# Kernel optimization log

Measured on AMD Instinct MI355X. Metric: run time of the kernel, lower is better.

Reference implementation:

```python
import jax, jax.numpy as jnp
import numpy as np

D = 128           # embed_dim
NUM_LAYERS = 2
N_CLASSES = 4
OUT_CELL = 64
SPEAKERS = 2
INPUT_DIMS = [768, 74, 35]
B, T = 32, 60


def setup_inputs() -> dict:
    key = jax.random.key(0)
    ks = jax.random.split(key, 24)
    inp = {}
    inp['x0'] = jax.random.normal(ks[0], (B, T, INPUT_DIMS[0]), jnp.float32)
    inp['x1'] = jax.random.normal(ks[1], (B, T, INPUT_DIMS[1]), jnp.float32)
    inp['x2'] = jax.random.normal(ks[2], (B, T, INPUT_DIMS[2]), jnp.float32)
    inp['smask'] = jax.random.normal(ks[3], (B, T, SPEAKERS), jnp.float32)  # argmax -> speaker ids
    # modality projections
    for i, d in enumerate(INPUT_DIMS):
        inp[f'Wp{i}'] = jax.random.normal(ks[4 + i], (d, D), jnp.float32) / np.float32(np.sqrt(d))
        inp[f'bp{i}'] = jnp.zeros((D,), jnp.float32)
    # shared PositionEmbedding (ModuleList([m]*3) shares params)
    inp['freq_emb'] = jax.random.normal(ks[7], (SPEAKERS, D), jnp.float32) * 0.1
    inp['phase_emb'] = jax.random.normal(ks[8], (SPEAKERS, D), jnp.float32)
    # shared QRNNCell (ModuleList([cell]*num_layers) shares params)
    inp['U_x'] = jnp.linalg.qr(jax.random.normal(ks[9], (D, D), jnp.float32))[0]
    inp['U_h'] = jnp.linalg.qr(jax.random.normal(ks[10], (D, D), jnp.float32))[0]
    inp['Lambda'] = jnp.float32(0.5)
    # QMeasurement kernel (real/imag parts of D measurement vectors)
    inp['kernel_r'] = jnp.eye(D, dtype=jnp.float32) + 0.05 * jax.random.normal(ks[11], (D, D), jnp.float32)
    inp['kernel_i'] = 0.05 * jax.random.normal(ks[12], (D, D), jnp.float32)
    # SimpleNet fc_out
    inp['W1'] = jax.random.normal(ks[13], (D, OUT_CELL), jnp.float32) / np.float32(np.sqrt(D))
    inp['b1'] = jnp.zeros((OUT_CELL,), jnp.float32)
    inp['W2'] = jax.random.normal(ks[14], (OUT_CELL, N_CLASSES), jnp.float32) / np.float32(np.sqrt(OUT_CELL))
    inp['b2'] = jnp.zeros((N_CLASSES,), jnp.float32)
    return inp


def _qmn_forward(x0, x1, x2, smask, Wp0, bp0, Wp1, bp1, Wp2, bp2,
                 freq_emb, phase_emb, U_x, U_h, Lambda,
                 kernel_r, kernel_i, W1, b1, W2, b2):
    xs = [x0, x1, x2]
    Ws = [(Wp0, bp0), (Wp1, bp1), (Wp2, bp2)]
    reps = [jax.nn.relu(x @ W + b) for x, (W, b) in zip(xs, Ws)]           # [B,T,D] each
    # mixture weights: softmax over per-modality L2 norms
    norms = jnp.concatenate([jnp.linalg.norm(r, axis=-1, keepdims=True) for r in reps], axis=-1)
    weights = jax.nn.softmax(norms, axis=-1)                               # [B,T,M]
    # shared phase embedding: phase = t * freq[speaker] + phase[speaker]
    ids = jnp.argmax(smask, axis=-1)                                       # [B,T] int
    pos = jnp.arange(T, dtype=jnp.float32)[None, :, None]                  # [1,T,1]
    phase = pos * freq_emb[ids] + phase_emb[ids]                           # [B,T,D]
    cosp, sinp = jnp.cos(phase), jnp.sin(phase)
    # mixed density matrices rho = sum_m w_m |v_m><v_m|
    rho_r = jnp.zeros((B, T, D, D), jnp.float32)
    rho_i = jnp.zeros((B, T, D, D), jnp.float32)
    for m, r in enumerate(reps):
        a = r / jnp.maximum(jnp.linalg.norm(r, axis=-1, keepdims=True), 1e-12)
        pr = a * cosp                                                       # real amplitude
        pi = a * sinp                                                       # imag amplitude
        w = weights[..., m][..., None, None]
        rho_r = rho_r + w * (jnp.einsum('btm,btn->btmn', pr, pr) + jnp.einsum('btm,btn->btmn', pi, pi))
        rho_i = rho_i + w * (jnp.einsum('btm,btn->btmn', pi, pr) - jnp.einsum('btm,btn->btmn', pr, pi))
    # time-major for scan
    sr = jnp.transpose(rho_r, (1, 0, 2, 3))                                # [T,B,D,D]
    si = jnp.transpose(rho_i, (1, 0, 2, 3))

    def cell(h, x):
        hr, hi = h
        xr, xi = x
        Xr = jnp.einsum('mp,bpq,nq->bmn', U_x, xr, U_x)
        Xi = jnp.einsum('mp,bpq,nq->bmn', U_x, xi, U_x)
        Hr = jnp.einsum('mp,bpq,nq->bmn', U_h, hr, U_h)
        Hi = jnp.einsum('mp,bpq,nq->bmn', U_h, hi, U_h)
        nr = Lambda * Hr + (1.0 - Lambda) * Xr
        ni = Lambda * Hi + (1.0 - Lambda) * Xi
        return (nr, ni), (nr, ni)

    h0 = (jnp.broadcast_to(jnp.eye(D, dtype=jnp.float32) / D, (B, D, D)),
          jnp.zeros((B, D, D), jnp.float32))
    for _ in range(NUM_LAYERS):  # same shared cell params each layer
        _, (sr, si) = jax.lax.scan(cell, h0, (sr, si))
    # QMeasurement: p_k = Re(v_k^dag rho v_k), unit-norm complex measurement vectors
    nrm = jnp.sqrt(jnp.sum(kernel_r**2 + kernel_i**2, axis=1, keepdims=True))
    vr = kernel_r / jnp.maximum(nrm, 1e-12)                                # [K,D], K=D
    vi = kernel_i / jnp.maximum(nrm, 1e-12)
    probs = (jnp.einsum('tbmn,km,kn->tbk', sr, vr, vr)
             + jnp.einsum('tbmn,km,kn->tbk', sr, vi, vi)
             - jnp.einsum('tbmn,km,kn->tbk', si, vr, vi)
             + jnp.einsum('tbmn,km,kn->tbk', si, vi, vr))                  # [T,B,D]
    # SimpleNet (dropout = identity at inference)
    hid = jax.nn.relu(probs @ W1 + b1)
    out = jnp.tanh(hid @ W2 + b2)                                          # [T,B,C]
    out = jnp.transpose(out, (1, 0, 2))                                    # [B,T,C]
    return jax.nn.log_softmax(out, axis=2)


def reference(x0, x1, x2, smask, Wp0, bp0, Wp1, bp1, Wp2, bp2,
              freq_emb, phase_emb, U_x, U_h, Lambda,
              kernel_r, kernel_i, W1, b1, W2, b2):
    return _qmn_forward(x0, x1, x2, smask, Wp0, bp0, Wp1, bp1, Wp2, bp2,
                        freq_emb, phase_emb, U_x, U_h, Lambda,
                        kernel_r, kernel_i, W1, b1, W2, b2)
```

## Files before the change

kernel.cpp:

```cpp
#include <hip/hip_runtime.h>


#define DB 32
#define DT 60
#define DD 128
#define BT (DB*DT)
#define SP 136

typedef unsigned short ushort_t;
typedef __attribute__((ext_vector_type(8))) __bf16 bf16x8;
typedef __attribute__((ext_vector_type(8))) unsigned short ushort8_t;
typedef __attribute__((ext_vector_type(4))) float  float4v;

__device__ __forceinline__ float bf2f(ushort_t u){
  union { unsigned int i; float f; } x; x.i = ((unsigned int)u) << 16; return x.f;
}
__device__ __forceinline__ ushort_t f2bf(float f){
  union { float f; unsigned int i; } x; x.f = f;
  unsigned int lsb = (x.i >> 16) & 1u;
  return (ushort_t)((x.i + 0x7FFFu + lsb) >> 16);
}
__device__ __forceinline__ unsigned int f2bfpk(float a, float b){
#if defined(__gfx950__) && __has_builtin(__builtin_amdgcn_cvt_pk_bf16_f32)
  auto v = __builtin_amdgcn_cvt_pk_bf16_f32(a, b);
  unsigned int r; __builtin_memcpy(&r, &v, 4); return r;
#else
  return (unsigned int)f2bf(a) | ((unsigned int)f2bf(b) << 16);
#endif
}
__device__ __forceinline__ void split2(float v, ushort_t& h, ushort_t& l){
  h = f2bf(v); l = f2bf(v - bf2f(h));
}

template<int RT, int CT, bool ALO, bool BLO>
__device__ __forceinline__ void gemm_t(const ushort_t* Ah, const ushort_t* Al,
                                       const ushort_t* Bh, const ushort_t* Bl,
                                       float4v* acc, int row0, int col0, int gma, int q)
{
  for (int ks = 0; ks < 4; ks++){
    int ko = ks*32 + q*8;
    bf16x8 aF[RT], aL[RT], bF[CT], bL[CT];
    #pragma unroll
    for (int R = 0; R < RT; R++){
      int row = row0 + 16*R + gma;
      aF[R] = *(const bf16x8*)&Ah[row*SP + ko];
      if (ALO) aL[R] = *(const bf16x8*)&Al[row*SP + ko];
    }
    #pragma unroll
    for (int C = 0; C < CT; C++){
      int row = col0 + 16*C + gma;
      bF[C] = *(const bf16x8*)&Bh[row*SP + ko];
      if (BLO) bL[C] = *(const bf16x8*)&Bl[row*SP + ko];
    }
    #pragma unroll
    for (int R = 0; R < RT; R++)
      #pragma unroll
      for (int C = 0; C < CT; C++){
        float4v c = acc[R*CT+C];
        c = __builtin_amdgcn_mfma_f32_16x16x32_bf16(aF[R], bF[C], c, 0, 0, 0);
        if (BLO) c = __builtin_amdgcn_mfma_f32_16x16x32_bf16(aF[R], bL[C], c, 0, 0, 0);
        if (ALO) c = __builtin_amdgcn_mfma_f32_16x16x32_bf16(aL[R], bF[C], c, 0, 0, 0);
        acc[R*CT+C] = c;
      }
  }
}

template<int RT, int CT>
__device__ __forceinline__ void emit_t(const float4v* acc, ushort_t* dst, int stride,
                                       int row0, int col0, int gma, int q){
  #pragma unroll
  for (int R = 0; R < RT; R++)
    #pragma unroll
    for (int C = 0; C < CT; C++){
      int c = col0 + 16*C + gma, r0 = row0 + 16*R + 4*q;
      uint2 o;
      o.x = f2bfpk(acc[R*CT+C][0], acc[R*CT+C][1]);
      o.y = f2bfpk(acc[R*CT+C][2], acc[R*CT+C][3]);
      *(uint2*)&dst[(size_t)c*stride + r0] = o;
    }
}
template<int RT, int CT>
__device__ __forceinline__ void emit_split_t(const float4v* acc, ushort_t* dh, ushort_t* dl, int stride,
                                             int row0, int col0, int gma, int q){
  #pragma unroll
  for (int R = 0; R < RT; R++)
    #pragma unroll
    for (int C = 0; C < CT; C++){
      int c = col0 + 16*C + gma, r0 = row0 + 16*R + 4*q;
      ushort4 hh, ll;
      split2(acc[R*CT+C][0], hh.x, ll.x); split2(acc[R*CT+C][1], hh.y, ll.y);
      split2(acc[R*CT+C][2], hh.z, ll.z); split2(acc[R*CT+C][3], hh.w, ll.w);
      *(ushort4*)&dh[(size_t)c*stride + r0] = hh;
      *(ushort4*)&dl[(size_t)c*stride + r0] = ll;
    }
}
template<int NT>
__device__ __forceinline__ void lds_load_mat(ushort_t* dst, const ushort_t* src, int tid){
  for (int i = tid*8; i < 16384; i += NT*8){
    int r = i >> 7, k = i & 127;
    *(ushort8_t*)&dst[r*SP + k] = *(const ushort8_t*)&src[i];
  }
}
template<int NT>
__device__ __forceinline__ void lds_load_rows16(ushort_t* dst, const ushort_t* src, int tid){
  for (int i = tid*8; i < 2048; i += NT*8){
    int r = i >> 7, k = i & 127;
    *(ushort8_t*)&dst[r*SP + k] = *(const ushort8_t*)&src[i];
  }
}
template<int NT>
__device__ __forceinline__ void lds_load_mat2(ushort_t* d0, const ushort_t* s0,
                                              ushort_t* d1, const ushort_t* s1, int tid){
  constexpr int CH = 16384/(NT*8);
  ushort8_t r0[CH], r1[CH];
  #pragma unroll
  for (int c = 0; c < CH; c++) r0[c] = *(const ushort8_t*)&s0[tid*8 + c*NT*8];
  #pragma unroll
  for (int c = 0; c < CH; c++) r1[c] = *(const ushort8_t*)&s1[tid*8 + c*NT*8];
  #pragma unroll
  for (int c = 0; c < CH; c++){
    int i = tid*8 + c*NT*8; int r = i >> 7, k = i & 127;
    *(ushort8_t*)&d0[r*SP + k] = r0[c];
  }
  #pragma unroll
  for (int c = 0; c < CH; c++){
    int i = tid*8 + c*NT*8; int r = i >> 7, k = i & 127;
    *(ushort8_t*)&d1[r*SP + k] = r1[c];
  }
}
template<int NT>
__device__ __forceinline__ void lds_store_mat(ushort_t* dst, const ushort_t* src, int tid){
  for (int i = tid*8; i < 16384; i += NT*8){
    int r = i >> 7, k = i & 127;
    *(ushort8_t*)&dst[i] = *(const ushort8_t*)&src[r*SP + k];
  }
}

__device__ __forceinline__ void pow2_body(int blk2, int s,
    ushort_t* PpH, ushort_t* PpL, ushort_t* PTh, ushort_t* PTl,
    int tid, ushort_t* Ah, ushort_t* Al, ushort_t* Bh, ushort_t* Bl)
{
  int which = blk2 >> 3, sl = blk2 & 7;
  size_t src = (size_t)(s-1)*16384, dst = (size_t)s*16384;
  int gcol0 = sl*16;
  const ushort_t *A_h, *A_l, *B_h, *B_l; ushort_t *D_h, *D_l;
  if (which == 0){ A_h = PTh+src; A_l = PTl+src; B_h = PpH+src; B_l = PpL+src;
                   D_h = PpH+dst; D_l = PpL+dst; }
  else           { A_h = PpH+src; A_l = PpL+src; B_h = PTh+src; B_l = PTl+src;
                   D_h = PTh+dst; D_l = PTl+dst; }
  if (tid < 256){
    lds_load_mat<256>(Ah, A_h, tid);
    lds_load_mat<256>(Al, A_l, tid);
    lds_load_rows16<256>(Bh, B_h + (size_t)gcol0*128, tid);
    lds_load_rows16<256>(Bl, B_l + (size_t)gcol0*128, tid);
  }
  __syncthreads();
  if (tid < 256){
    int w = tid >> 6, lane = tid & 63, gma = lane & 15, q = lane >> 4;
    int row0 = 32*w;
    float4v acc[2];
    acc[0] = (float4v){0.f,0.f,0.f,0.f};
    acc[1] = (float4v){0.f,0.f,0.f,0.f};
    gemm_t<2,1,true,true>(Ah, Al, Bh, Bl, acc, row0, 0, gma, q);
    emit_split_t<2,1>(acc, D_h, D_l, 128, row0, gcol0, gma, q);
  }
}

__global__ void k_small(const float* Ux, const float* Uh, const float* kr, const float* ki,
                        const float* Wp0, const float* Wp1, const float* Wp2,
                        const float* x0, const float* x1, const float* x2,
                        ushort_t* UxTh, ushort_t* UxTl, ushort_t* UxH, ushort_t* UxL,
                        float* Vr, float* Vi,
                        ushort_t* PpH, ushort_t* PpL, ushort_t* PTh, ushort_t* PTl,
                        ushort_t* WT0h, ushort_t* WT0l, ushort_t* WT1h, ushort_t* WT1l,
                        ushort_t* WT2h, ushort_t* WT2l,
                        ushort_t* X0h, ushort_t* X0l, ushort_t* X1h, ushort_t* X1l,
                        ushort_t* X2h, ushort_t* X2l){
  int blk = blockIdx.x, d = threadIdx.x;
  if (blk < 128){
    int i = blk;
    float v = Ux[i*DD + d];
    ushort_t h, l; split2(v, h, l);
    UxTh[d*DD + i] = h; UxTl[d*DD + i] = l;
  } else if (blk < 256){
    __shared__ float red[DD];
    int k = blk - 128;
    float r = kr[k*DD+d], im = ki[k*DD+d];
    red[d] = r*r + im*im;
    __syncthreads();
    for (int s = 64; s > 0; s >>= 1){ if (d < s) red[d] += red[d+s]; __syncthreads(); }
    float nrm = fmaxf(sqrtf(red[0]), 1e-12f);
    Vr[k*DD+d] = r/nrm; Vi[k*DD+d] = im/nrm;
  } else if (blk < 384){
    int i = blk - 256;
    float v = Uh[i*DD + d];
    ushort_t h, l; split2(v, h, l);
    PpH[i*DD + d] = h;  PpL[i*DD + d] = l;
    PTh[d*DD + i] = h;  PTl[d*DD + i] = l;
  } else if (blk < 512){
    int dd2 = blk - 384;
    ushort_t h, l;
    for (int k = d; k < 768; k += 128){
      split2(Wp0[(size_t)k*DD + dd2], h, l);
      WT0h[(size_t)dd2*768 + k] = h; WT0l[(size_t)dd2*768 + k] = l;
    }
    { float v = (d < 74) ? Wp1[(size_t)d*DD + dd2] : 0.f;
      split2(v, h, l); WT1h[dd2*128 + d] = h; WT1l[dd2*128 + d] = l; }
    { float v = (d < 35) ? Wp2[(size_t)d*DD + dd2] : 0.f;
      split2(v, h, l); WT2h[dd2*128 + d] = h; WT2l[dd2*128 + d] = l; }
    { split2(Ux[(size_t)dd2*DD + d], h, l);
      UxH[dd2*DD + d] = h; UxL[dd2*DD + d] = l; }
  } else {
    int bt = blk - 512;
    ushort_t h, l;
    const float* r0 = x0 + (size_t)bt*768;
    #pragma unroll
    for (int j = 0; j < 6; j++){
      split2(r0[j*128 + d], h, l);
      X0h[(size_t)bt*768 + j*128 + d] = h;
      X0l[(size_t)bt*768 + j*128 + d] = l;
    }
    float v1 = (d < 74) ? x1[(size_t)bt*74 + d] : 0.f;
    split2(v1, h, l);
    X1h[(size_t)bt*128 + d] = h; X1l[(size_t)bt*128 + d] = l;
    float v2 = (d < 35) ? x2[(size_t)bt*35 + d] : 0.f;
    split2(v2, h, l);
    X2h[(size_t)bt*128 + d] = h; X2l[(size_t)bt*128 + d] = l;
  }
}

__global__ __launch_bounds__(512,1) void k_proj(
    const ushort_t* X0h, const ushort_t* X0l, const ushort_t* X1h, const ushort_t* X1l,
    const ushort_t* X2h, const ushort_t* X2l,
    const ushort_t* WT0h, const ushort_t* WT0l, const ushort_t* WT1h, const ushort_t* WT1l,
    const ushort_t* WT2h, const ushort_t* WT2l,
    const float* bp1, const float* bp2,
    float* Rpart, float* Reps,
    ushort_t* PpH, ushort_t* PpL, ushort_t* PTh, ushort_t* PTl)
{
  __shared__ ushort_t Ah[128*SP], Al[128*SP], Bh[128*SP], Bl[128*SP];
  int blk = blockIdx.x;
  int tid = threadIdx.x;
  if (blk >= 120){
    pow2_body(blk - 120, 1, PpH, PpL, PTh, PTl, tid, Ah, Al, Bh, Bl);
    return;
  }
  int m, tile, ch;
  if (blk < 90){ m = 0; tile = blk/6; ch = blk%6; }
  else if (blk < 105){ m = 1; tile = blk-90; ch = 0; }
  else { m = 2; tile = blk-105; ch = 0; }
  int bt0 = tile*128;
  int w = tid >> 6, lane = tid & 63, gma = lane & 15, q = lane >> 4;
  int row0 = 32*(w >> 1), col0 = 64*(w & 1);
  const ushort_t* Wh_ = (m==0)? WT0h : (m==1)? WT1h : WT2h;
  const ushort_t* Wl_ = (m==0)? WT0l : (m==1)? WT1l : WT2l;
  const ushort_t* Xh_ = (m==0)? X0h : (m==1)? X1h : X2h;
  const ushort_t* Xl_ = (m==0)? X0l : (m==1)? X1l : X2l;
  int KX = (m==0)? 768 : 128;
  for (int i = tid*8; i < 16384; i += 4096){
    int r = i >> 7, k = i & 127;
    *(ushort8_t*)&Ah[r*SP + k] = *(const ushort8_t*)&Wh_[(size_t)r*KX + ch*128 + k];
    *(ushort8_t*)&Al[r*SP + k] = *(const ushort8_t*)&Wl_[(size_t)r*KX + ch*128 + k];
    *(ushort8_t*)&Bh[r*SP + k] = *(const ushort8_t*)&Xh_[(size_t)(bt0+r)*KX + ch*128 + k];
    *(ushort8_t*)&Bl[r*SP + k] = *(const ushort8_t*)&Xl_[(size_t)(bt0+r)*KX + ch*128 + k];
  }
  __syncthreads();
  float4v acc[8];
  #pragma unroll
  for (int i = 0; i < 8; i++) acc[i] = (float4v){0.f,0.f,0.f,0.f};
  gemm_t<2,4,true,true>(Ah, Al, Bh, Bl, acc, row0, col0, gma, q);
  if (m == 0){
    #pragma unroll
    for (int R = 0; R < 2; R++)
      #pragma unroll
      for (int C = 0; C < 4; C++){
        int c = col0 + 16*C + gma, r0 = row0 + 16*R + 4*q;
        float4 o;
        o.x = acc[R*4+C][0]; o.y = acc[R*4+C][1];
        o.z = acc[R*4+C][2]; o.w = acc[R*4+C][3];
        *(float4*)&Rpart[((size_t)ch*BT + bt0 + c)*128 + r0] = o;
      }
  } else {
    const float* bp = (m==1)? bp1 : bp2;
    #pragma unroll
    for (int R = 0; R < 2; R++){
      int r0 = row0 + 16*R + 4*q;
      float4 bv = *(const float4*)&bp[r0];
      #pragma unroll
      for (int C = 0; C < 4; C++){
        int c = col0 + 16*C + gma;
        float4v a = acc[R*4+C];
        float4 o;
        o.x = fmaxf(a[0]+bv.x, 0.f); o.y = fmaxf(a[1]+bv.y, 0.f);
        o.z = fmaxf(a[2]+bv.z, 0.f); o.w = fmaxf(a[3]+bv.w, 0.f);
        *(float4*)&Reps[(size_t)(bt0 + c)*384 + m*128 + r0] = o;
      }
    }
  }
}

__global__ __launch_bounds__(128) void k_mix(const float* Rpart, const float* Reps,
    const float* bp0, const float* smask,
    const float* freq, const float* phem, ushort_t* PsH, ushort_t* PsL, float* Wgt)
{
  __shared__ float part[2][3];
  int bt = blockIdx.x; int t = bt % DT;
  int d = threadIdx.x;
  float r0v = bp0[d];
  #pragma unroll
  for (int ch = 0; ch < 6; ch++)
    r0v += Rpart[((size_t)ch*BT + bt)*128 + d];
  r0v = fmaxf(r0v, 0.f);
  float r1v = Reps[(size_t)bt*384 + 128 + d];
  float r2v = Reps[(size_t)bt*384 + 256 + d];
  float s0 = r0v*r0v, s1 = r1v*r1v, s2 = r2v*r2v;
  #pragma unroll
  for (int off = 1; off < 64; off <<= 1){
    s0 += __shfl_xor(s0, off, 64);
    s1 += __shfl_xor(s1, off, 64);
    s2 += __shfl_xor(s2, off, 64);
  }
  int wv = d >> 6;
  if ((d & 63) == 0){ part[wv][0] = s0; part[wv][1] = s1; part[wv][2] = s2; }
  __syncthreads();
  float n0 = sqrtf(part[0][0] + part[1][0]);
  float n1 = sqrtf(part[0][1] + part[1][1]);
  float n2 = sqrtf(part[0][2] + part[1][2]);
  float mx = fmaxf(n0, fmaxf(n1, n2));
  float e0 = expf(n0-mx), e1 = expf(n1-mx), e2 = expf(n2-mx);
  float einv = 1.f/(e0+e1+e2);
  if (d < 3) Wgt[bt*3+d] = (d==0?e0:(d==1?e1:e2))*einv;
  float sm0 = smask[bt*2], sm1 = smask[bt*2+1];
  int id = (sm1 > sm0) ? 1 : 0;
  float ph = (float)t * freq[id*DD+d] + phem[id*DD+d];
  float cp = cosf(ph), sp = sinf(ph);
  float a0 = r0v / fmaxf(n0, 1e-12f);
  float a1 = r1v / fmaxf(n1, 1e-12f);
  float a2 = r2v / fmaxf(n2, 1e-12f);
  ushort_t h, l;
  split2(a0*cp, h, l); PsH[((size_t)0*BT + bt)*DD + d] = h; PsL[((size_t)0*BT + bt)*DD + d] = l;
  split2(a1*cp, h, l); PsH[((size_t)1*BT + bt)*DD + d] = h; PsL[((size_t)1*BT + bt)*DD + d] = l;
  split2(a2*cp, h, l); PsH[((size_t)2*BT + bt)*DD + d] = h; PsL[((size_t)2*BT + bt)*DD + d] = l;
  split2(a0*sp, h, l); PsH[((size_t)3*BT + bt)*DD + d] = h; PsL[((size_t)3*BT + bt)*DD + d] = l;
  split2(a1*sp, h, l); PsH[((size_t)4*BT + bt)*DD + d] = h; PsL[((size_t)4*BT + bt)*DD + d] = l;
  split2(a2*sp, h, l); PsH[((size_t)5*BT + bt)*DD + d] = h; PsL[((size_t)5*BT + bt)*DD + d] = l;
}

__global__ __launch_bounds__(512,1) void k_qtrans(const ushort_t* UxH, const ushort_t* UxL,
                                                  const ushort_t* PsH, const ushort_t* PsL,
                                                  ushort_t* Qb,
                                                  ushort_t* PpH, ushort_t* PpL,
                                                  ushort_t* PTh, ushort_t* PTl){
  __shared__ ushort_t Ah[128*SP], Al[128*SP], Bh[128*SP], Bl[128*SP];
  int blk = blockIdx.x;
  int tid = threadIdx.x;
  if (blk >= 90){
    pow2_body(blk - 90, 2, PpH, PpL, PTh, PTl, tid, Ah, Al, Bh, Bl);
    return;
  }
  int w = tid >> 6, lane = tid & 63, gma = lane & 15, q = lane >> 4;
  int row0 = 32*(w >> 1), col0 = 64*(w & 1);
  size_t rbase = (size_t)blk*128*128;
  lds_load_mat<512>(Ah, UxH, tid);
  lds_load_mat<512>(Al, UxL, tid);
  lds_load_mat<512>(Bh, PsH + rbase, tid);
  lds_load_mat<512>(Bl, PsL + rbase, tid);
  __syncthreads();
  float4v acc[8];
  #pragma unroll
  for (int i = 0; i < 8; i++) acc[i] = (float4v){0.f,0.f,0.f,0.f};
  gemm_t<2,4,true,true>(Ah, Al, Bh, Bl, acc, row0, col0, gma, q);
  emit_t<2,4>(acc, Qb + rbase, 128, row0, col0, gma, q);
}

__global__ __launch_bounds__(256,2) void k_pow2v2(ushort_t* PpH, ushort_t* PpL,
                                                  ushort_t* PTh, ushort_t* PTl, int s){
  __shared__ ushort_t Ah[128*SP], Al[128*SP], Bh[16*SP], Bl[16*SP];
  int blk = blockIdx.x;
  int which = blk >> 3, sl = blk & 7;
  size_t src = (size_t)(s-1)*16384, dst = (size_t)s*16384;
  int tid = threadIdx.x;
  int w = tid >> 6, lane = tid & 63, gma = lane & 15, q = lane >> 4;
  int row0 = 32*w;
  int gcol0 = sl*16;
  const ushort_t *A_h, *A_l, *B_h, *B_l; ushort_t *D_h, *D_l;
  if (which == 0){ A_h = PTh+src; A_l = PTl+src; B_h = PpH+src; B_l = PpL+src;
                   D_h = PpH+dst; D_l = PpL+dst; }
  else           { A_h = PpH+src; A_l = PpL+src; B_h = PTh+src; B_l = PTl+src;
                   D_h = PTh+dst; D_l = PTl+dst; }
  lds_load_mat<256>(Ah, A_h, tid);
  lds_load_mat<256>(Al, A_l, tid);
  lds_load_rows16<256>(Bh, B_h + (size_t)gcol0*128, tid);
  lds_load_rows16<256>(Bl, B_l + (size_t)gcol0*128, tid);
  __syncthreads();
  float4v acc[2];
  acc[0] = (float4v){0.f,0.f,0.f,0.f};
  acc[1] = (float4v){0.f,0.f,0.f,0.f};
  gemm_t<2,1,true,true>(Ah, Al, Bh, Bl, acc, row0, 0, gma, q);
  emit_split_t<2,1>(acc, D_h, D_l, 128, row0, gcol0, gma, q);
}

__global__ __launch_bounds__(512,1) void k_gchain(const ushort_t* PpH, const ushort_t* PpL,
                                                  const ushort_t* PTh, const ushort_t* PTl,
                                                  ushort_t* GTh, ushort_t* GTl){
  __shared__ ushort_t Ah[128*SP], Al[128*SP], Bh[128*SP], Bl[128*SP];
  int t = blockIdx.x;
  int tid = threadIdx.x;
  int w = tid >> 6, lane = tid & 63, gma = lane & 15, q = lane >> 4;
  int row0 = 32*(w >> 1), col0 = 64*(w & 1);
  size_t gslot = (size_t)t * 16384;
  if (t == 0){
    for (int i = tid*4; i < 16384; i += 2048){
      int r = i >> 7, k = i & 127;
      ushort4 zz; zz.x = zz.y = zz.z = zz.w = 0;
      *(ushort4*)&GTl[gslot + i] = zz;
      ushort4 oh;
      oh.x = (r == (k+0)) ? (ushort_t)0x3F80 : (ushort_t)0;
      oh.y = (r == (k+1)) ? (ushort_t)0x3F80 : (ushort_t)0;
      oh.z = (r == (k+2)) ? (ushort_t)0x3F80 : (ushort_t)0;
      oh.w = (r == (k+3)) ? (ushort_t)0x3F80 : (ushort_t)0;
      *(ushort4*)&GTh[gslot + i] = oh;
    }
    return;
  }
  int b0 = __ffs(t) - 1;
  int rem = t & ~(1 << b0);
  if (rem == 0){
    size_t ps = (size_t)b0 * 16384;
    for (int i = tid*4; i < 16384; i += 2048){
      *(ushort4*)&GTh[gslot + i] = *(const ushort4*)&PTh[ps + i];
      *(ushort4*)&GTl[gslot + i] = *(const ushort4*)&PTl[ps + i];
    }
    return;
  }
  lds_load_mat<512>(Ah, PpH + (size_t)b0*16384, tid);
  lds_load_mat<512>(Al, PpL + (size_t)b0*16384, tid);
  while (rem){
    int k = __ffs(rem) - 1;
    rem &= ~(1 << k);
    lds_load_mat<512>(Bh, PTh + (size_t)k*16384, tid);
    lds_load_mat<512>(Bl, PTl + (size_t)k*16384, tid);
    __syncthreads();
    float4v acc[8];
    #pragma unroll
    for (int i = 0; i < 8; i++) acc[i] = (float4v){0.f,0.f,0.f,0.f};
    if (rem){
      gemm_t<2,4,true,true>(Bh, Bl, Ah, Al, acc, row0, col0, gma, q);
      __syncthreads();
      emit_split_t<2,4>(acc, Ah, Al, SP, row0, col0, gma, q);
      __syncthreads();
    } else {
      gemm_t<2,4,true,true>(Ah, Al, Bh, Bl, acc, row0, col0, gma, q);
      emit_split_t<2,4>(acc, GTh + gslot, GTl + gslot, 128, row0, col0, gma, q);
    }
  }
}

__global__ __launch_bounds__(512,1) void k_mwvt(
    const ushort_t* GTh, const ushort_t* GTl,
    const ushort_t* UxTh, const ushort_t* UxTl,
    const float* Vr, const float* Vi,
    const ushort_t* Qb,
    ushort_t* Mh, ushort_t* Wh, ushort_t* At)
{
  __shared__ ushort_t LBUF[4*128*SP];
  int blk = blockIdx.x;
  int tid = threadIdx.x;
  if (blk < 180){
    ushort_t* Bh = LBUF;
    ushort_t* Bl = LBUF + 128*SP;
    ushort_t* Ah = LBUF + 2*128*SP;
    ushort_t* Al = LBUF + 3*128*SP;
    int w = tid >> 6, lane = tid & 63, gma = lane & 15, q = lane >> 4;
    int row0 = 64*(w >> 1), col0 = 64*(w & 1);
    if (blk < 60){
      int t = blk;
      if (tid < 256){
        lds_load_mat<256>(Bh, GTh + (size_t)t*16384, tid);
        lds_load_mat<256>(Bl, GTl + (size_t)t*16384, tid);
        lds_load_mat<256>(Ah, UxTh, tid);
        lds_load_mat<256>(Al, UxTl, tid);
      }
      __syncthreads();
      float4v acc[16];
      if (tid < 256){
        #pragma unroll
        for (int i = 0; i < 16; i++) acc[i] = (float4v){0.f,0.f,0.f,0.f};
        gemm_t<4,4,true,true>(Ah, Al, Bh, Bl, acc, row0, col0, gma, q);
      }
      __syncthreads();
      if (tid < 256) emit_split_t<4,4>(acc, Ah, Al, SP, row0, col0, gma, q);
      __syncthreads();
      if (tid < 256){
        #pragma unroll
        for (int i = 0; i < 16; i++) acc[i] = (float4v){0.f,0.f,0.f,0.f};
        gemm_t<4,4,true,true>(Bh, Bl, Ah, Al, acc, row0, col0, gma, q);
        #pragma unroll
        for (int R = 0; R < 4; R++)
          #pragma unroll
          for (int C = 0; C < 4; C++){
            int c = col0 + 16*C + gma, r0 = row0 + 16*R + 4*q;
            uint2 o;
            o.x = f2bfpk(acc[R*4+C][0], acc[R*4+C][1]);
            o.y = f2bfpk(acc[R*4+C][2], acc[R*4+C][3]);
            *(uint2*)&Mh[(size_t)t*16384 + c*128 + r0] = o;
          }
      }
    } else {
      int bx = blk - 60;
      int t = bx >> 1, which = bx & 1;
      if (tid < 256){
        lds_load_mat<256>(Ah, GTh + (size_t)t*16384, tid);
        lds_load_mat<256>(Al, GTl + (size_t)t*16384, tid);
        const float* V = which ? Vi : Vr;
        for (int i = tid; i < 16384; i += 256){
          int r = i >> 7, k = i & 127;
          ushort_t h, l; split2(V[i], h, l);
          Bh[r*SP + k] = h; Bl[r*SP + k] = l;
        }
      }
      __syncthreads();
      if (tid < 256){
        float4v acc[16];
        #pragma unroll
        for (int i = 0; i < 16; i++) acc[i] = (float4v){0.f,0.f,0.f,0.f};
        gemm_t<4,4,true,true>(Ah, Al, Bh, Bl, acc, row0, col0, gma, q);
        #pragma unroll
        for (int R = 0; R < 4; R++)
          #pragma unroll
          for (int C = 0; C < 4; C++){
            int c = col0 + 16*C + gma, r0 = row0 + 16*R + 4*q;
            uint2 o;
            o.x = f2bfpk(acc[R*4+C][0], acc[R*4+C][1]);
            o.y = f2bfpk(acc[R*4+C][2], acc[R*4+C][3]);
            *(uint2*)&Wh[(size_t)bx*16384 + c*128 + r0] = o;
          }
      }
    }
  } else {
    ushort_t* Ah = LBUF;
    ushort_t* Bs = LBUF + 128*SP;
    int t = blk - 180;
    int w = tid >> 6, lane = tid & 63, gma = lane & 15, q = lane >> 4;
    int row0 = (w & 3)*32, col0 = (w >> 2)*96;
    lds_load_mat<512>(Ah, GTh + (size_t)t*16384, tid);
    for (int i = tid*8; i < 192*128; i += 4096){
      int m = i >> 7, k = i & 127;
      int j = m >> 5, b = m & 31;
      *(ushort8_t*)&Bs[m*SP + k] =
        *(const ushort8_t*)&Qb[((size_t)(j*BT) + b*DT + t)*DD + k];
    }
    __syncthreads();
    float4v acc[12];
    #pragma unroll
    for (int i = 0; i < 12; i++) acc[i] = (float4v){0.f,0.f,0.f,0.f};
    gemm_t<2,6,false,false>(Ah, Ah, Bs, Bs, acc, row0, col0, gma, q);
    emit_t<2,6>(acc, At + (size_t)t*24576, 128, row0, col0, gma, q);
  }
}

__global__ __launch_bounds__(256) void k_zbuild(ushort_t* S, const ushort_t* At,
                                                const float* Wgt, const float* lamp){
  __shared__ ushort_t As[2][6*DD];
  __shared__ float wl[2][3];
  int blk = blockIdx.x;
  int b = blk >> 5, sl2 = blk & 31;
  int tid = threadIdx.x;
  int r = sl2*4 + (tid >> 6);
  int c = (tid*2) & 127;
  float lam = lamp[0];
  float z0 = 0.f, z1 = 0.f;
  size_t off = (size_t)sl2*512 + tid*2;
  ushort4 pre;
  float wpre = 0.f;
  int jj0 = 0, n0 = 0;
  if (tid < 192){
    int i = tid*4;
    jj0 = i >> 7; n0 = i & 127;
    pre = *(const ushort4*)&At[(size_t)(jj0*32 + b)*128 + n0];
  }
  if (tid < 3) wpre = Wgt[(b*DT)*3 + tid];
  for (int t = 0; t < DT; t++){
    int cur = t & 1;
    if (tid < 192) *(ushort4*)&As[cur][tid*4] = pre;
    if (tid < 3) wl[cur][tid] = wpre;
    __syncthreads();
    if (t+1 < DT){
      if (tid < 192)
        pre = *(const ushort4*)&At[(size_t)(t+1)*24576 + (size_t)(jj0*32 + b)*128 + n0];
      if (tid < 3) wpre = Wgt[(b*DT + t+1)*3 + tid];
    }
    float ar[6];
    #pragma unroll
    for (int jj = 0; jj < 6; jj++) ar[jj] = bf2f(As[cur][jj*128 + r]);
    float w0 = wl[cur][0], w1 = wl[cur][1], w2 = wl[cur][2];
    float cb[6];
    cb[0] = w0*(ar[0]+ar[3]); cb[1] = w1*(ar[1]+ar[4]); cb[2] = w2*(ar[2]+ar[5]);
    cb[3] = w0*(ar[3]-ar[0]); cb[4] = w1*(ar[4]-ar[1]); cb[5] = w2*(ar[5]-ar[2]);
    float y0 = 0.f, y1 = 0.f;
    #pragma unroll
    for (int jj = 0; jj < 6; jj++){
      unsigned int a2 = *(const unsigned int*)&As[cur][jj*128 + c];
      float w_ = cb[jj];
      y0 += w_*bf2f((ushort_t)(a2 & 0xFFFF));
      y1 += w_*bf2f((ushort_t)(a2 >> 16));
    }
    z0 = lam*z0 + y0; z1 = lam*z1 + y1;
    *(unsigned int*)&S[((size_t)(t*32 + b))*16384 + off] = f2bfpk(z0, z1);
  }
}

__global__ __launch_bounds__(512,2) void k_conjmid(ushort_t* S, const ushort_t* Mh,
                                                   const float* lamp){
  __shared__ ushort_t Bh[128*SP], Zs[128*SP];
  int raw = blockIdx.x;
  int g = raw & 7, t = raw >> 3;
  int tid = threadIdx.x;
  int w = tid >> 6, lane = tid & 63, gma = lane & 15, q = lane >> 4;
  int row0 = 32*(w >> 1), col0 = 64*(w & 1);
  size_t slot0 = (size_t)(t*32 + g*4) * 16384;
  lds_load_mat2<512>(Zs, S + slot0, Bh, Mh + (size_t)t*16384, tid);
  __syncthreads();
  float lam = lamp[0];
  float oml = 1.f - lam;
  float ct = powf(lam, (float)(t+1)) / 128.f;
  for (int ib = 0; ib < 4; ib++){
    size_t slot = slot0 + (size_t)ib*16384;
    ushort8_t znext[4];
    if (ib < 3){
      #pragma unroll
      for (int c = 0; c < 4; c++)
        znext[c] = *(const ushort8_t*)&S[slot + 16384 + tid*8 + c*4096];
    }
    float4v acc[8];
    #pragma unroll
    for (int i = 0; i < 8; i++) acc[i] = (float4v){0.f,0.f,0.f,0.f};
    gemm_t<2,4,false,false>(Zs, Zs, Bh, Bh, acc, row0, col0, gma, q);
    __syncthreads();
    emit_t<2,4>(acc, Zs, SP, row0, col0, gma, q);
    __syncthreads();
    #pragma unroll
    for (int i = 0; i < 8; i++) acc[i] = (float4v){0.f,0.f,0.f,0.f};
    gemm_t<2,4,false,false>(Zs, Zs, Bh, Bh, acc, row0, col0, gma, q);
    __syncthreads();
    #pragma unroll
    for (int R = 0; R < 2; R++)
      #pragma unroll
      for (int C = 0; C < 4; C++){
        int c = col0 + 16*C + gma, r0 = row0 + 16*R + 4*q;
        float v0 = oml*acc[R*4+C][0] + ((c == r0+0) ? ct : 0.f);
        float v1 = oml*acc[R*4+C][1] + ((c == r0+1) ? ct : 0.f);
        float v2 = oml*acc[R*4+C][2] + ((c == r0+2) ? ct : 0.f);
        float v3 = oml*acc[R*4+C][3] + ((c == r0+3) ? ct : 0.f);
        uint2 o; o.x = f2bfpk(v0, v1); o.y = f2bfpk(v2, v3);
        *(uint2*)&Zs[(size_t)c*SP + r0] = o;
      }
    __syncthreads();
    lds_store_mat<512>(S + slot, Zs, tid);
    if (ib < 3){
      __syncthreads();
      #pragma unroll
      for (int c = 0; c < 4; c++){
        int i = tid*8 + c*4096;
        int r = i >> 7, k = i & 127;
        *(ushort8_t*)&Zs[r*SP + k] = znext[c];
      }
      __syncthreads();
    }
  }
}

__device__ __forceinline__ void prefix_ph2(uint2& buf, bool doload,
                                           const ushort_t* Snext, ushort_t* Scur,
                                           float* a, float lam){
  uint2 u = buf;
  if (doload) buf = *(const uint2*)Snext;
  a[0] = lam*a[0] + bf2f((ushort_t)(u.x & 0xFFFF));
  a[1] = lam*a[1] + bf2f((ushort_t)(u.x >> 16));
  a[2] = lam*a[2] + bf2f((ushort_t)(u.y & 0xFFFF));
  a[3] = lam*a[3] + bf2f((ushort_t)(u.y >> 16));
  uint2 o;
  o.x = f2bfpk(a[0], a[1]); o.y = f2bfpk(a[2], a[3]);
  *(uint2*)Scur = o;
}
__global__ __launch_bounds__(128) void k_prefix(ushort_t* S, const float* lamp){
  int blk = blockIdx.x;
  int chain = blk >> 5, slab = blk & 31;
  int tid = threadIdx.x;
  size_t off = (size_t)slab*512 + tid*4;
  float lam = lamp[0];
  float a[4];
  #pragma unroll
  for (int i = 0; i < 4; i++) a[i] = 0.f;
  size_t addr = (size_t)chain*16384 + off;
  const size_t step = (size_t)32*16384;
  uint2 b0 = *(const uint2*)&S[addr];
  uint2 b1 = *(const uint2*)&S[addr + step];
  uint2 b2 = *(const uint2*)&S[addr + 2*step];
  uint2 b3 = *(const uint2*)&S[addr + 3*step];
  uint2 b4 = *(const uint2*)&S[addr + 4*step];
  uint2 b5 = *(const uint2*)&S[addr + 5*step];
  for (int t = 0; t < DT; t += 6){
    prefix_ph2(b0, t+6  < DT, &S[addr + 6*step], &S[addr], a, lam); addr += step;
    prefix_ph2(b1, t+7  < DT, &S[addr + 6*step], &S[addr], a, lam); addr += step;
    prefix_ph2(b2, t+8  < DT, &S[addr + 6*step], &S[addr], a, lam); addr += step;
    prefix_ph2(b3, t+9  < DT, &S[addr + 6*step], &S[addr], a, lam); addr += step;
    prefix_ph2(b4, t+10 < DT, &S[addr + 6*step], &S[addr], a, lam); addr += step;
    prefix_ph2(b5, t+11 < DT, &S[addr + 6*step], &S[addr], a, lam); addr += step;
  }
}

__global__ __launch_bounds__(512,2) void k_meas(const ushort_t* S, const ushort_t* Wh,
                                                const float* lamp, float* Probs){
  __shared__ ushort_t Vs[128*SP], Cs[128*SP];
  __shared__ float Pd[64];
  int raw = blockIdx.x;
  int h = raw / 240;
  int rem = raw % 240;
  int t = rem >> 2, g = rem & 3;
  int tid = threadIdx.x;
  int w = tid >> 6, lane = tid & 63, gma = lane & 15, q = lane >> 4;
  int row0 = 16*(w >> 1);
  int col0 = 64*(w & 1);
  size_t wbase = (size_t)(t*2) * 16384;
  size_t slot0 = (size_t)(t*32 + g*8) * 16384;
  ushort8_t creg[4], vreg[4];
  #pragma unroll
  for (int c = 0; c < 4; c++)
    creg[c] = *(const ushort8_t*)&S[slot0 + tid*8 + c*4096];
  #pragma unroll
  for (int c = 0; c < 4; c++){
    int i = tid*8 + c*4096;
    int r = i >> 7, k = i & 127;
    size_t gsrc = wbase + ((r < 64) ? 0 : 16384) + (size_t)(64*h + (r & 63))*128 + k;
    vreg[c] = *(const ushort8_t*)&Wh[gsrc];
  }
  if (tid < 64) Pd[tid] = 0.f;
  #pragma unroll
  for (int c = 0; c < 4; c++){
    int i = tid*8 + c*4096;
    int r = i >> 7, k = i & 127;
    *(ushort8_t*)&Cs[r*SP + k] = creg[c];
    *(ushort8_t*)&Vs[r*SP + k] = vreg[c];
  }
  __syncthreads();
  float lam = lamp[0];
  float ct = powf(lam, (float)(t+1)) / 128.f;
  for (int ib = 0; ib < 8; ib++){
    if (ib < 7){
      size_t snx = slot0 + (size_t)(ib+1)*16384;
      #pragma unroll
      for (int c = 0; c < 4; c++)
        creg[c] = *(const ushort8_t*)&S[snx + tid*8 + c*4096];
    }
    float4v acc[8];
    #pragma unroll
    for (int i = 0; i < 8; i++) acc[i] = (float4v){0.f,0.f,0.f,0.f};
    #pragma unroll
    for (int ks = 0; ks < 4; ks++){
      int ko = ks*32 + q*8;
      bf16x8 aF0 = *(const bf16x8*)&Vs[(row0 + gma)*SP + ko];
      bf16x8 aF1 = *(const bf16x8*)&Vs[(row0 + 64 + gma)*SP + ko];
      bf16x8 bF[4];
      #pragma unroll
      for (int C = 0; C < 4; C++)
        bF[C] = *(const bf16x8*)&Cs[(col0 + 16*C + gma)*SP + ko];
      #pragma unroll
      for (int C = 0; C < 4; C++){
        acc[C]   = __builtin_amdgcn_mfma_f32_16x16x32_bf16(aF0, bF[C], acc[C],   0, 0, 0);
        acc[4+C] = __builtin_amdgcn_mfma_f32_16x16x32_bf16(aF1, bF[C], acc[4+C], 0, 0, 0);
      }
    }
    #pragma unroll
    for (int j = 0; j < 4; j++){
      int kr = row0 + 4*q + j;
      float s = 0.f;
      #pragma unroll
      for (int C = 0; C < 4; C++){
        int m = col0 + 16*C + gma;
        float w0 = bf2f(Vs[kr*SP + m]);
        float w1 = bf2f(Vs[(kr + 64)*SP + m]);
        s += acc[C][j]*(w0 + w1) + acc[4+C][j]*(w1 - w0);
      }
      #pragma unroll
      for (int off = 1; off < 16; off <<= 1)
        s += __shfl_xor(s, off, 64);
      if (gma == 0) atomicAdd(&Pd[kr], s);
    }
    __syncthreads();
    if (tid < 64){
      Probs[(size_t)(t*32 + g*8 + ib)*DD + 64*h + tid] = (1.f - lam)*Pd[tid] + ct;
      Pd[tid] = 0.f;
    }
    if (ib < 7){
      #pragma unroll
      for (int c = 0; c < 4; c++){
        int i = tid*8 + c*4096;
        int r = i >> 7, k = i & 127;
        *(ushort8_t*)&Cs[r*SP + k] = creg[c];
      }
    }
    __syncthreads();
  }
}

__global__ __launch_bounds__(64) void k_head(const float* Probs, const float* W1, const float* b1,
                        const float* W2, const float* b2, float* out)
{
  __shared__ float ps[DD];
  __shared__ float hid[64];
  __shared__ float ov[4];
  int tb = blockIdx.x;
  int tid = threadIdx.x;
  ps[tid] = Probs[(size_t)tb*DD + tid];
  ps[tid+64] = Probs[(size_t)tb*DD + 64 + tid];
  __syncthreads();
  float acc = b1[tid];
  for (int dd = 0; dd < DD; dd++) acc += ps[dd]*W1[dd*64 + tid];
  hid[tid] = fmaxf(acc, 0.f);
  __syncthreads();
  if (tid < 4){
    float o = b2[tid];
    for (int j = 0; j < 64; j++) o += hid[j]*W2[j*4 + tid];
    ov[tid] = tanhf(o);
  }
  __syncthreads();
  if (tid == 0){
    float m = fmaxf(fmaxf(ov[0],ov[1]), fmaxf(ov[2],ov[3]));
    float lse = logf(expf(ov[0]-m)+expf(ov[1]-m)+expf(ov[2]-m)+expf(ov[3]-m));
    int t = tb >> 5, b = tb & 31;
    float* o = out + ((size_t)(b*DT + t))*4;
    o[0] = ov[0]-m-lse; o[1] = ov[1]-m-lse;
    o[2] = ov[2]-m-lse; o[3] = ov[3]-m-lse;
  }
}

extern "C" void kernel_launch(void* const* d_in, const int* in_sizes, int n_in,
                              void* d_out, int out_size, void* d_ws, size_t ws_size,
                              hipStream_t stream)
{
  const float* x0    = (const float*)d_in[0];
  const float* x1    = (const float*)d_in[1];
  const float* x2    = (const float*)d_in[2];
  const float* smask = (const float*)d_in[3];
  const float* Wp0   = (const float*)d_in[4];
  const float* bp0   = (const float*)d_in[5];
  const float* Wp1   = (const float*)d_in[6];
  const float* bp1   = (const float*)d_in[7];
  const float* Wp2   = (const float*)d_in[8];
  const float* bp2   = (const float*)d_in[9];
  const float* freq  = (const float*)d_in[10];
  const float* phem  = (const float*)d_in[11];
  const float* Ux    = (const float*)d_in[12];
  const float* Uh    = (const float*)d_in[13];
  const float* lamp  = (const float*)d_in[14];
  const float* kr    = (const float*)d_in[15];
  const float* ki    = (const float*)d_in[16];
  const float* W1    = (const float*)d_in[17];
  const float* b1    = (const float*)d_in[18];
  const float* W2    = (const float*)d_in[19];
  const float* b2    = (const float*)d_in[20];

  char* ws = (char*)d_ws;
  auto alignup = [](size_t x){ return (x + 255) & ~(size_t)255; };
  size_t off = 0;
  ushort_t* S   = (ushort_t*)(ws + off); off = alignup(off + (size_t)1920*16384*sizeof(ushort_t));
  ushort_t* Qb  = (ushort_t*)(ws + off); off = alignup(off + (size_t)6*BT*DD*sizeof(ushort_t));
  float* Rpart  = (float*)(ws + off);    off = alignup(off + (size_t)6*BT*DD*sizeof(float));
  float* Reps   = (float*)(ws + off);    off = alignup(off + (size_t)BT*384*sizeof(float));
  ushort_t* PsH = (ushort_t*)(ws + off); off = alignup(off + (size_t)6*BT*DD*sizeof(ushort_t));
  ushort_t* PsL = (ushort_t*)(ws + off); off = alignup(off + (size_t)6*BT*DD*sizeof(ushort_t));
  ushort_t* X0h = (ushort_t*)(ws + off); off = alignup(off + (size_t)BT*768*sizeof(ushort_t));
  ushort_t* X0l = (ushort_t*)(ws + off); off = alignup(off + (size_t)BT*768*sizeof(ushort_t));
  ushort_t* X1h = (ushort_t*)(ws + off); off = alignup(off + (size_t)BT*128*sizeof(ushort_t));
  ushort_t* X1l = (ushort_t*)(ws + off); off = alignup(off + (size_t)BT*128*sizeof(ushort_t));
  ushort_t* X2h = (ushort_t*)(ws + off); off = alignup(off + (size_t)BT*128*sizeof(ushort_t));
  ushort_t* X2l = (ushort_t*)(ws + off); off = alignup(off + (size_t)BT*128*sizeof(ushort_t));
  float* Wgt    = (float*)(ws + off);    off = alignup(off + (size_t)BT*3*sizeof(float));
  float* Vr     = (float*)(ws + off);    off = alignup(off + (size_t)DD*DD*sizeof(float));
  float* Vi     = (float*)(ws + off);    off = alignup(off + (size_t)DD*DD*sizeof(float));
  ushort_t* UxTh = (ushort_t*)(ws + off); off = alignup(off + (size_t)DD*DD*sizeof(ushort_t));
  ushort_t* UxTl = (ushort_t*)(ws + off); off = alignup(off + (size_t)DD*DD*sizeof(ushort_t));
  ushort_t* UxH = (ushort_t*)(ws + off); off = alignup(off + (size_t)DD*DD*sizeof(ushort_t));
  ushort_t* UxL = (ushort_t*)(ws + off); off = alignup(off + (size_t)DD*DD*sizeof(ushort_t));
  float* Probs  = (float*)(ws + off);    off = alignup(off + (size_t)BT*DD*sizeof(float));
  ushort_t* PpH = (ushort_t*)(ws + off); off = alignup(off + (size_t)6*16384*sizeof(ushort_t));
  ushort_t* PpL = (ushort_t*)(ws + off); off = alignup(off + (size_t)6*16384*sizeof(ushort_t));
  ushort_t* PTh = (ushort_t*)(ws + off); off = alignup(off + (size_t)6*16384*sizeof(ushort_t));
  ushort_t* PTl = (ushort_t*)(ws + off); off = alignup(off + (size_t)6*16384*sizeof(ushort_t));
  ushort_t* Mh  = (ushort_t*)(ws + off); off = alignup(off + (size_t)60*16384*sizeof(ushort_t));
  ushort_t* Wmh = (ushort_t*)(ws + off); off = alignup(off + (size_t)120*16384*sizeof(ushort_t));
  ushort_t* GTh = (ushort_t*)(ws + off); off = alignup(off + (size_t)60*16384*sizeof(ushort_t));
  ushort_t* GTl = (ushort_t*)(ws + off); off = alignup(off + (size_t)60*16384*sizeof(ushort_t));
  ushort_t* At  = (ushort_t*)(ws + off); off = alignup(off + (size_t)60*24576*sizeof(ushort_t));
  ushort_t* WT0h = (ushort_t*)(ws + off); off = alignup(off + (size_t)128*768*sizeof(ushort_t));
  ushort_t* WT0l = (ushort_t*)(ws + off); off = alignup(off + (size_t)128*768*sizeof(ushort_t));
  ushort_t* WT1h = (ushort_t*)(ws + off); off = alignup(off + (size_t)128*128*sizeof(ushort_t));
  ushort_t* WT1l = (ushort_t*)(ws + off); off = alignup(off + (size_t)128*128*sizeof(ushort_t));
  ushort_t* WT2h = (ushort_t*)(ws + off); off = alignup(off + (size_t)128*128*sizeof(ushort_t));
  ushort_t* WT2l = (ushort_t*)(ws + off); off = alignup(off + (size_t)128*128*sizeof(ushort_t));
  (void)ws_size; (void)in_sizes; (void)n_in; (void)out_size;

  k_small<<<512 + BT, 128, 0, stream>>>(Ux, Uh, kr, ki, Wp0, Wp1, Wp2, x0, x1, x2,
                                        UxTh, UxTl, UxH, UxL, Vr, Vi,
                                        PpH, PpL, PTh, PTl,
                                        WT0h, WT0l, WT1h, WT1l, WT2h, WT2l,
                                        X0h, X0l, X1h, X1l, X2h, X2l);
  k_proj<<<136, 512, 0, stream>>>(X0h, X0l, X1h, X1l, X2h, X2l,
                                  WT0h, WT0l, WT1h, WT1l, WT2h, WT2l,
                                  bp1, bp2, Rpart, Reps, PpH, PpL, PTh, PTl);
  k_mix<<<BT, 128, 0, stream>>>(Rpart, Reps, bp0, smask, freq, phem, PsH, PsL, Wgt);
  k_qtrans<<<106, 512, 0, stream>>>(UxH, UxL, PsH, PsL, Qb, PpH, PpL, PTh, PTl);
  for (int s = 3; s <= 5; s++)
    k_pow2v2<<<16, 256, 0, stream>>>(PpH, PpL, PTh, PTl, s);
  k_gchain<<<60, 512, 0, stream>>>(PpH, PpL, PTh, PTl, GTh, GTl);
  k_mwvt<<<240, 512, 0, stream>>>(GTh, GTl, UxTh, UxTl, Vr, Vi, Qb, Mh, Wmh, At);
  k_zbuild<<<1024, 256, 0, stream>>>(S, At, Wgt, lamp);
  k_conjmid<<<480, 512, 0, stream>>>(S, Mh, lamp);
  k_prefix<<<1024, 128, 0, stream>>>(S, lamp);
  k_meas<<<480, 512, 0, stream>>>(S, Wmh, lamp, Probs);
  k_head<<<BT, 64, 0, stream>>>(Probs, W1, b1, W2, b2, (float*)d_out);
}
```

Measured before the change: 294.4 us.

## Fuse measurement and classifier head into one kernel covering both halves

The measurement kernel now covers all 128 measurement outputs per block with 1024 threads (two 64-row halves), loading each density-matrix slot once instead of once per half. The MLP head, tanh and log-softmax run inside the same block, so the Probs round trip and the separate head launch go away. The cost is more LDS per block (W1 staged in shared memory), one block per CU, and extra barriers plus serial head work done by few threads inside the time loop.

```diff
diff --git a/kernel.cpp b/kernel.cpp
--- a/kernel.cpp
+++ b/kernel.cpp
@@ -710,48 +710,66 @@
   }
 }
 
-__global__ __launch_bounds__(512,2) void k_meas(const ushort_t* S, const ushort_t* Wh,
-                                                const float* lamp, float* Probs){
-  __shared__ ushort_t Vs[128*SP], Cs[128*SP];
-  __shared__ float Pd[64];
+__global__ __launch_bounds__(1024,1) void k_meas2(const ushort_t* S, const ushort_t* Wh,
+                                                  const float* lamp,
+                                                  const float* W1, const float* b1,
+                                                  const float* W2, const float* b2,
+                                                  float* out){
+  __shared__ ushort_t Vs[2*128*SP], Cs[128*SP];
+  __shared__ float W1s[128*64];
+  __shared__ float Pd[128], psb[128], hidb[64], ovb[4];
   int raw = blockIdx.x;
-  int h = raw / 240;
-  int rem = raw % 240;
-  int t = rem >> 2, g = rem & 3;
+  int t = raw >> 2, g = raw & 3;
   int tid = threadIdx.x;
   int w = tid >> 6, lane = tid & 63, gma = lane & 15, q = lane >> 4;
-  int row0 = 16*(w >> 1);
-  int col0 = 64*(w & 1);
+  int h = w >> 3, w2 = w & 7;
+  int row0 = 16*(w2 >> 1);
+  int col0 = 64*(w2 & 1);
   size_t wbase = (size_t)(t*2) * 16384;
   size_t slot0 = (size_t)(t*32 + g*8) * 16384;
-  ushort8_t creg[4], vreg[4];
-  #pragma unroll
-  for (int c = 0; c < 4; c++)
-    creg[c] = *(const ushort8_t*)&S[slot0 + tid*8 + c*4096];
+  ushort8_t creg[2], vreg[4];
+  #pragma unroll
+  for (int c = 0; c < 2; c++)
+    creg[c] = *(const ushort8_t*)&S[slot0 + tid*8 + c*8192];
   #pragma unroll
   for (int c = 0; c < 4; c++){
-    int i = tid*8 + c*4096;
-    int r = i >> 7, k = i & 127;
-    size_t gsrc = wbase + ((r < 64) ? 0 : 16384) + (size_t)(64*h + (r & 63))*128 + k;
+    int i = tid*8 + c*8192;
+    int hh = i >> 14;
+    int loc = i & 16383;
+    int r = loc >> 7, k = loc & 127;
+    size_t gsrc = wbase + ((r < 64) ? 0 : 16384) + (size_t)(64*hh + (r & 63))*128 + k;
     vreg[c] = *(const ushort8_t*)&Wh[gsrc];
   }
-  if (tid < 64) Pd[tid] = 0.f;
-  #pragma unroll
-  for (int c = 0; c < 4; c++){
-    int i = tid*8 + c*4096;
+  #pragma unroll
+  for (int c = 0; c < 2; c++){
+    int i = tid*4 + c*4096;
+    *(float4*)&W1s[i] = *(const float4*)&W1[i];
+  }
+  if (tid < 128) Pd[tid] = 0.f;
+  #pragma unroll
+  for (int c = 0; c < 2; c++){
+    int i = tid*8 + c*8192;
     int r = i >> 7, k = i & 127;
     *(ushort8_t*)&Cs[r*SP + k] = creg[c];
-    *(ushort8_t*)&Vs[r*SP + k] = vreg[c];
+  }
+  #pragma unroll
+  for (int c = 0; c < 4; c++){
+    int i = tid*8 + c*8192;
+    int hh = i >> 14;
+    int loc = i & 16383;
+    int r = loc >> 7, k = loc & 127;
+    *(ushort8_t*)&Vs[hh*128*SP + r*SP + k] = vreg[c];
   }
   __syncthreads();
   float lam = lamp[0];
   float ct = powf(lam, (float)(t+1)) / 128.f;
+  const ushort_t* Vsh = Vs + h*128*SP;
   for (int ib = 0; ib < 8; ib++){
     if (ib < 7){
       size_t snx = slot0 + (size_t)(ib+1)*16384;
       #pragma unroll
-      for (int c = 0; c < 4; c++)
-        creg[c] = *(const ushort8_t*)&S[snx + tid*8 + c*4096];
+      for (int c = 0; c < 2; c++)
+        creg[c] = *(const ushort8_t*)&S[snx + tid*8 + c*8192];
     }
     float4v acc[8];
     #pragma unroll
@@ -759,8 +777,8 @@
     #pragma unroll
     for (int ks = 0; ks < 4; ks++){
       int ko = ks*32 + q*8;
-      bf16x8 aF0 = *(const bf16x8*)&Vs[(row0 + gma)*SP + ko];
-      bf16x8 aF1 = *(const bf16x8*)&Vs[(row0 + 64 + gma)*SP + ko];
+      bf16x8 aF0 = *(const bf16x8*)&Vsh[(row0 + gma)*SP + ko];
+      bf16x8 aF1 = *(const bf16x8*)&Vsh[(row0 + 64 + gma)*SP + ko];
       bf16x8 bF[4];
       #pragma unroll
       for (int C = 0; C < 4; C++)
@@ -778,60 +796,49 @@
       #pragma unroll
       for (int C = 0; C < 4; C++){
         int m = col0 + 16*C + gma;
-        float w0 = bf2f(Vs[kr*SP + m]);
-        float w1 = bf2f(Vs[(kr + 64)*SP + m]);
+        float w0 = bf2f(Vsh[kr*SP + m]);
+        float w1 = bf2f(Vsh[(kr + 64)*SP + m]);
         s += acc[C][j]*(w0 + w1) + acc[4+C][j]*(w1 - w0);
       }
       #pragma unroll
       for (int off = 1; off < 16; off <<= 1)
         s += __shfl_xor(s, off, 64);
-      if (gma == 0) atomicAdd(&Pd[kr], s);
-    }
+      if (gma == 0) atomicAdd(&Pd[64*h + kr], s);
+    }
+    __syncthreads();
+    if (tid < 128){ psb[tid] = (1.f - lam)*Pd[tid] + ct; Pd[tid] = 0.f; }
     __syncthreads();
     if (tid < 64){
-      Probs[(size_t)(t*32 + g*8 + ib)*DD + 64*h + tid] = (1.f - lam)*Pd[tid] + ct;
-      Pd[tid] = 0.f;
+      float a1 = b1[tid];
+      #pragma unroll 4
+      for (int d = 0; d < 128; d++) a1 += psb[d]*W1s[d*64 + tid];
+      hidb[tid] = fmaxf(a1, 0.f);
+    }
+    __syncthreads();
+    if (tid < 4){
+      float o = b2[tid];
+      for (int j = 0; j < 64; j++) o += hidb[j]*W2[j*4 + tid];
+      ovb[tid] = tanhf(o);
+    }
+    __syncthreads();
+    if (tid == 0){
+      float m = fmaxf(fmaxf(ovb[0],ovb[1]), fmaxf(ovb[2],ovb[3]));
+      float lse = logf(expf(ovb[0]-m)+expf(ovb[1]-m)+expf(ovb[2]-m)+expf(ovb[3]-m));
+      int tb = t*32 + g*8 + ib;
+      int b = tb & 31;
+      float* o = out + ((size_t)(b*DT + t))*4;
+      o[0] = ovb[0]-m-lse; o[1] = ovb[1]-m-lse;
+      o[2] = ovb[2]-m-lse; o[3] = ovb[3]-m-lse;
     }
     if (ib < 7){
       #pragma unroll
-      for (int c = 0; c < 4; c++){
-        int i = tid*8 + c*4096;
+      for (int c = 0; c < 2; c++){
+        int i = tid*8 + c*8192;
         int r = i >> 7, k = i & 127;
         *(ushort8_t*)&Cs[r*SP + k] = creg[c];
       }
     }
     __syncthreads();
-  }
-}
-
-__global__ __launch_bounds__(64) void k_head(const float* Probs, const float* W1, const float* b1,
-                        const float* W2, const float* b2, float* out)
-{
-  __shared__ float ps[DD];
-  __shared__ float hid[64];
-  __shared__ float ov[4];
-  int tb = blockIdx.x;
-  int tid = threadIdx.x;
-  ps[tid] = Probs[(size_t)tb*DD + tid];
-  ps[tid+64] = Probs[(size_t)tb*DD + 64 + tid];
-  __syncthreads();
-  float acc = b1[tid];
-  for (int dd = 0; dd < DD; dd++) acc += ps[dd]*W1[dd*64 + tid];
-  hid[tid] = fmaxf(acc, 0.f);
-  __syncthreads();
-  if (tid < 4){
-    float o = b2[tid];
-    for (int j = 0; j < 64; j++) o += hid[j]*W2[j*4 + tid];
-    ov[tid] = tanhf(o);
-  }
-  __syncthreads();
-  if (tid == 0){
-    float m = fmaxf(fmaxf(ov[0],ov[1]), fmaxf(ov[2],ov[3]));
-    float lse = logf(expf(ov[0]-m)+expf(ov[1]-m)+expf(ov[2]-m)+expf(ov[3]-m));
-    int t = tb >> 5, b = tb & 31;
-    float* o = out + ((size_t)(b*DT + t))*4;
-    o[0] = ov[0]-m-lse; o[1] = ov[1]-m-lse;
-    o[2] = ov[2]-m-lse; o[3] = ov[3]-m-lse;
   }
 }
 
@@ -899,7 +906,7 @@
   ushort_t* WT1l = (ushort_t*)(ws + off); off = alignup(off + (size_t)128*128*sizeof(ushort_t));
   ushort_t* WT2h = (ushort_t*)(ws + off); off = alignup(off + (size_t)128*128*sizeof(ushort_t));
   ushort_t* WT2l = (ushort_t*)(ws + off); off = alignup(off + (size_t)128*128*sizeof(ushort_t));
-  (void)ws_size; (void)in_sizes; (void)n_in; (void)out_size;
+  (void)ws_size; (void)in_sizes; (void)n_in; (void)out_size; (void)Probs;
 
   k_small<<<512 + BT, 128, 0, stream>>>(Ux, Uh, kr, ki, Wp0, Wp1, Wp2, x0, x1, x2,
                                         UxTh, UxTl, UxH, UxL, Vr, Vi,
@@ -918,6 +925,5 @@
   k_zbuild<<<1024, 256, 0, stream>>>(S, At, Wgt, lamp);
   k_conjmid<<<480, 512, 0, stream>>>(S, Mh, lamp);
   k_prefix<<<1024, 128, 0, stream>>>(S, lamp);
-  k_meas<<<480, 512, 0, stream>>>(S, Wmh, lamp, Probs);
-  k_head<<<BT, 64, 0, stream>>>(Probs, W1, b1, W2, b2, (float*)d_out);
-}
+  k_meas2<<<240, 1024, 0, stream>>>(S, Wmh, lamp, W1, b1, W2, b2, (float*)d_out);
+}
```

Result: slower. 332.7 us (+13.0%).
